# Performance work log

Measured on AMD Instinct MI355X. Metric: run time of the kernel, lower is better.

Reference implementation:

```python
import jax, jax.numpy as jnp
import numpy as np

B, C, H, W = 8, 64, 64, 64
CQK = C // 8

def setup_inputs() -> dict:
    key = jax.random.key(0)
    ks = jax.random.split(key, 8)
    s = 0.05
    return {
        "X": jax.random.normal(ks[0], (B, C, H, W), dtype=jnp.float32),
        "Wq": jax.random.normal(ks[1], (CQK, C), dtype=jnp.float32) * s,
        "bq": jax.random.normal(ks[2], (CQK,), dtype=jnp.float32) * s,
        "Wk": jax.random.normal(ks[3], (CQK, C), dtype=jnp.float32) * s,
        "bk": jax.random.normal(ks[4], (CQK,), dtype=jnp.float32) * s,
        "Wv": jax.random.normal(ks[5], (C, C), dtype=jnp.float32) * s,
        "bv": jax.random.normal(ks[6], (C,), dtype=jnp.float32) * s,
        "gamma": jax.random.normal(ks[7], (1,), dtype=jnp.float32) * 0.5,
    }

def reference(X, Wq, bq, Wk, bk, Wv, bv, gamma):
    b, c, h, w = X.shape
    n = h * w
    Xf = X.reshape(b, c, n)  # [B, C, N]
    # 1x1 convs == per-pixel linear over channels
    q = jnp.einsum('oc,bcn->bno', Wq, Xf) + bq            # [B, N, Cqk]
    k = jnp.einsum('oc,bcn->bon', Wk, Xf) + bk[:, None]    # [B, Cqk, N]
    v = jnp.einsum('oc,bcn->bon', Wv, Xf) + bv[:, None]    # [B, C, N]
    energy = jnp.einsum('bnd,bdm->bnm', q, k)              # [B, N, N] (no scale, as in source)
    attention = jax.nn.softmax(energy, axis=-1)
    out = jnp.einsum('bcn,bmn->bcm', v, attention)         # value @ attention^T
    out = out.reshape(b, c, h, w)
    return X + out * gamma[0]
```

## Files before the change

### kernel.cpp

```cpp
#include <hip/hip_runtime.h>
#include <hip/hip_bf16.h>

#define BB 8
#define CC 64
#define NN 4096
#define LOG2E 1.44269504088896340736f

typedef short bf16x8 __attribute__((ext_vector_type(8)));
typedef float f32x16 __attribute__((ext_vector_type(16)));
typedef unsigned int uint4v __attribute__((ext_vector_type(4)));

__device__ __forceinline__ unsigned cvt_pk_bf16(float lo, float hi) {
    unsigned r;
    asm("v_cvt_pk_bf16_f32 %0, %1, %2" : "=v"(r) : "v"(lo), "v"(hi));
    return r;
}

__device__ __forceinline__ float fast_exp2(float x) {
#if __has_builtin(__builtin_amdgcn_exp2f)
    return __builtin_amdgcn_exp2f(x);
#else
    return __builtin_exp2f(x);
#endif
}


__global__ __launch_bounds__(256) void qkv_kernel(
    const float* __restrict__ X,
    const float* __restrict__ Wq, const float* __restrict__ bq,
    const float* __restrict__ Wk, const float* __restrict__ bk,
    const float* __restrict__ Wv, const float* __restrict__ bv,
    unsigned short* __restrict__ qw, unsigned short* __restrict__ kfrag,
    unsigned short* __restrict__ vfrag)
{
    __shared__ float wbuf[64 * 16];
    __shared__ float bsh[16];
    __shared__ short vsh[16][264];

    const int t = threadIdx.x;
    const int grp = blockIdx.x % 5;
    const int tile = blockIdx.x / 5;
    const int b = tile >> 4;
    const int nb = (tile & 15) << 8;
    const int n = nb + t;

    if (grp == 0) {
        for (int i = t; i < 512; i += 256) {
            int o = i >> 6, c = i & 63;
            wbuf[c * 16 + o]     = Wq[i];
            wbuf[c * 16 + 8 + o] = Wk[i];
        }
        if (t < 8) { bsh[t] = bq[t]; bsh[8 + t] = bk[t]; }
    } else {
        const int cbase = (grp - 1) * 16;
        for (int i = t; i < 1024; i += 256) {
            int o = i >> 6, c = i & 63;
            wbuf[c * 16 + o] = Wv[(cbase + o) * 64 + c];
        }
        if (t < 16) bsh[t] = bv[cbase + t];
    }
    __syncthreads();

    float a[16];
    #pragma unroll
    for (int j = 0; j < 16; j++) a[j] = bsh[j];

    const float* xp = X + (size_t)b * CC * NN + n;
    for (int c = 0; c < 64; c++) {
        float xc = xp[(size_t)c * NN];
        const float4* w4 = (const float4*)&wbuf[c * 16];
        float4 w0 = w4[0], w1 = w4[1], w2 = w4[2], w3 = w4[3];
        a[0]  += w0.x * xc; a[1]  += w0.y * xc; a[2]  += w0.z * xc; a[3]  += w0.w * xc;
        a[4]  += w1.x * xc; a[5]  += w1.y * xc; a[6]  += w1.z * xc; a[7]  += w1.w * xc;
        a[8]  += w2.x * xc; a[9]  += w2.y * xc; a[10] += w2.z * xc; a[11] += w2.w * xc;
        a[12] += w3.x * xc; a[13] += w3.y * xc; a[14] += w3.z * xc; a[15] += w3.w * xc;
    }

    if (grp == 0) {
        alignas(16) __hip_bfloat16 qb8[8], kb8[8];
        #pragma unroll
        for (int d = 0; d < 8; d++) {
            qb8[d] = __float2bfloat16(a[d] * LOG2E);
            kb8[d] = __float2bfloat16(a[8 + d]);
        }
        const size_t g = (size_t)b * NN + n;
        *(int4*)(qw + g * 8) = *(const int4*)qb8;
        size_t kf = ((size_t)b * 128 + (n >> 5)) * 512;
        *(int4*)(kfrag + kf + (size_t)(n & 31) * 8) = *(const int4*)kb8;
        *(int4*)(kfrag + kf + (size_t)(32 + (n & 31)) * 8) = make_int4(0, 0, 0, 0);
    } else {
        const int cbase = (grp - 1) * 16;
        const int qb0 = cbase & 31, ct = cbase >> 5;
        #pragma unroll
        for (int j = 0; j < 16; j++)
            vsh[j][t] = __builtin_bit_cast(short, __float2bfloat16(a[j]));
        __syncthreads();
        #pragma unroll
        for (int rr = 0; rr < 2; ++rr) {
            int r = 2 * t + rr;
            int qq = r & 15, hh = (r >> 4) & 1, gg = (r >> 5) & 3, tau = r >> 7;
            int n0 = tau * 64 + gg * 16 + hh * 8;
            int4 val = *(const int4*)&vsh[qq][n0];
            int gtile = (nb >> 6) + tau;
            size_t dst = ((size_t)(b * 64 + gtile)) * 4096
                       + (size_t)(gg * 2 + ct) * 512
                       + (size_t)(32 * hh + qb0 + qq) * 8;
            *(int4*)(vfrag + dst) = val;
        }
    }
}

template<int KS, bool FUSE>
__global__ __launch_bounds__(256, 2) void attn_kernel(
    const unsigned short* __restrict__ qw,
    const unsigned short* __restrict__ kfrag,
    const unsigned short* __restrict__ vfrag,
    unsigned short* __restrict__ pout, float* __restrict__ pl,
    const float* __restrict__ X, const float* __restrict__ gamma,
    float* __restrict__ out)
{
    const int t = threadIdx.x;
    const int w = t >> 6, lane = t & 63;
    const int h = lane >> 5, q = lane & 31;

    const int nwg = gridDim.x;
    const int cpx = nwg >> 3;
    const int bid = (blockIdx.x & 7) * cpx + (blockIdx.x >> 3);

    const int qtile = bid & 15;
    const int b = (bid >> 4) & 7;
    const int ks = bid >> 7;

    const int qbase = qtile * 256 + w * 64;

    bf16x8 qfA = {}, qfB = {};
    if (h == 0) {
        qfA = *(const bf16x8*)(qw + ((size_t)b * NN + qbase + q) * 8);
        qfB = *(const bf16x8*)(qw + ((size_t)b * NN + qbase + 32 + q) * 8);
    }

    f32x16 accA0 = {}, accA1 = {}, accB0 = {}, accB1 = {};
    float lsumA = 0.f, lsumB = 0.f;

    const int NT = NN / KS / 64;
    const unsigned short* kb = kfrag + (size_t)b * 65536
                             + (size_t)ks * NT * 1024 + (size_t)lane * 8;
    const unsigned short* vbp = vfrag + (size_t)b * 262144
                              + (size_t)ks * NT * 4096 + (size_t)lane * 8;

    auto phase = [&](const f32x16& sA, const f32x16& sB,
                     bf16x8 va, bf16x8 vb2, bf16x8 vc, bf16x8 vd) {
        float pa[16], pb[16];
        #pragma unroll
        for (int r = 0; r < 16; ++r) { pa[r] = fast_exp2(sA[r]); pb[r] = fast_exp2(sB[r]); }
        {
            float a0 = 0.f, a1 = 0.f, b0 = 0.f, b1 = 0.f;
            #pragma unroll
            for (int r = 0; r < 8; ++r) {
                a0 += pa[r]; a1 += pa[8 + r];
                b0 += pb[r]; b1 += pb[8 + r];
            }
            lsumA += a0 + a1;
            lsumB += b0 + b1;
        }
        unsigned ka[8], kb2[8];
        #pragma unroll
        for (int j = 0; j < 8; ++j) {
            ka[j]  = cvt_pk_bf16(pa[2 * j], pa[2 * j + 1]);
            kb2[j] = cvt_pk_bf16(pb[2 * j], pb[2 * j + 1]);
        }
        __builtin_amdgcn_s_setprio(1);
        #pragma unroll
        for (int g2 = 0; g2 < 2; ++g2) {
            const unsigned* pga = &ka[4 * g2];
            auto ra = __builtin_amdgcn_permlane32_swap(pga[2], pga[0], false, false);
            auto rb = __builtin_amdgcn_permlane32_swap(pga[3], pga[1], false, false);
            uint4v bua = { ra[1], rb[1], ra[0], rb[0] };
            bf16x8 pfA = __builtin_bit_cast(bf16x8, bua);
            const unsigned* pgb = &kb2[4 * g2];
            auto rc = __builtin_amdgcn_permlane32_swap(pgb[2], pgb[0], false, false);
            auto rd = __builtin_amdgcn_permlane32_swap(pgb[3], pgb[1], false, false);
            uint4v bub = { rc[1], rd[1], rc[0], rd[0] };
            bf16x8 pfB = __builtin_bit_cast(bf16x8, bub);

            bf16x8 vx = g2 ? vc : va;
            bf16x8 vy = g2 ? vd : vb2;
            accA0 = __builtin_amdgcn_mfma_f32_32x32x16_bf16(vx, pfA, accA0, 0, 0, 0);
            accA1 = __builtin_amdgcn_mfma_f32_32x32x16_bf16(vy, pfA, accA1, 0, 0, 0);
            accB0 = __builtin_amdgcn_mfma_f32_32x32x16_bf16(vx, pfB, accB0, 0, 0, 0);
            accB1 = __builtin_amdgcn_mfma_f32_32x32x16_bf16(vy, pfB, accB1, 0, 0, 0);
        }
        __builtin_amdgcn_s_setprio(0);
    };

    bf16x8 kc0 = *(const bf16x8*)kb;
    bf16x8 kc1 = *(const bf16x8*)(kb + 512);

    for (int it = 0; it < NT; ++it) {
        const unsigned short* vp = vbp + (size_t)it * 4096;
        bf16x8 v0 = *(const bf16x8*)(vp);
        bf16x8 v1 = *(const bf16x8*)(vp + 512);
        bf16x8 v2 = *(const bf16x8*)(vp + 1024);
        bf16x8 v3 = *(const bf16x8*)(vp + 1536);
        bf16x8 v4 = *(const bf16x8*)(vp + 2048);
        bf16x8 v5 = *(const bf16x8*)(vp + 2560);
        bf16x8 v6 = *(const bf16x8*)(vp + 3072);
        bf16x8 v7 = *(const bf16x8*)(vp + 3584);

        const int nit = (it + 1 < NT) ? it + 1 : it;
        const unsigned short* knp = kb + (size_t)nit * 1024;
        bf16x8 kn0 = *(const bf16x8*)knp;
        bf16x8 kn1 = *(const bf16x8*)(knp + 512);

        {
            f32x16 sA = __builtin_amdgcn_mfma_f32_32x32x16_bf16(kc0, qfA, (f32x16){}, 0, 0, 0);
            f32x16 sB = __builtin_amdgcn_mfma_f32_32x32x16_bf16(kc0, qfB, (f32x16){}, 0, 0, 0);
            phase(sA, sB, v0, v1, v2, v3);
        }
        {
            f32x16 sA = __builtin_amdgcn_mfma_f32_32x32x16_bf16(kc1, qfA, (f32x16){}, 0, 0, 0);
            f32x16 sB = __builtin_amdgcn_mfma_f32_32x32x16_bf16(kc1, qfB, (f32x16){}, 0, 0, 0);
            phase(sA, sB, v4, v5, v6, v7);
        }
        kc0 = kn0;
        kc1 = kn1;
    }

    auto rsA = __builtin_amdgcn_permlane32_swap(__builtin_bit_cast(unsigned, lsumA),
                                                __builtin_bit_cast(unsigned, lsumA), false, false);
    float ltotA = __builtin_bit_cast(float, rsA[0]) + __builtin_bit_cast(float, rsA[1]);
    auto rsB = __builtin_amdgcn_permlane32_swap(__builtin_bit_cast(unsigned, lsumB),
                                                __builtin_bit_cast(unsigned, lsumB), false, false);
    float ltotB = __builtin_bit_cast(float, rsB[0]) + __builtin_bit_cast(float, rsB[1]);

    const float gm = FUSE ? gamma[0] : 0.f;

    #pragma unroll
    for (int sub = 0; sub < 2; ++sub) {
        const int n = qbase + sub * 32 + q;
        const float ltot = sub ? ltotB : ltotA;
        const f32x16& a0 = sub ? accB0 : accA0;
        const f32x16& a1 = sub ? accB1 : accA1;
        if (FUSE) {
            const float inv = 1.f / ltot;
            #pragma unroll
            for (int ct = 0; ct < 2; ++ct) {
                const f32x16& a = ct ? a1 : a0;
                #pragma unroll
                for (int r = 0; r < 16; ++r) {
                    int c = ct * 32 + (r & 3) + 8 * (r >> 2) + 4 * h;
                    size_t idx = ((size_t)(b * CC + c)) * NN + n;
                    out[idx] = X[idx] + gm * a[r] * inv;
                }
            }
        } else {
            unsigned short* po = pout + (size_t)ks * BB * CC * NN;
            #pragma unroll
            for (int ct = 0; ct < 2; ++ct) {
                const f32x16& a = ct ? a1 : a0;
                #pragma unroll
                for (int r = 0; r < 16; ++r) {
                    int c = ct * 32 + (r & 3) + 8 * (r >> 2) + 4 * h;
                    po[((size_t)(b * CC + c)) * NN + n] =
                        __builtin_bit_cast(unsigned short, __float2bfloat16(a[r]));
                }
            }
            if (h == 0) pl[((size_t)(ks * BB + b)) * NN + n] = ltot;
        }
    }
}

template<int KS>
__global__ __launch_bounds__(256) void combine_kernel(
    const unsigned short* __restrict__ pout, const float* __restrict__ pl,
    const float* __restrict__ X, const float* __restrict__ gamma,
    float* __restrict__ out)
{
    const int idx = blockIdx.x * 256 + threadIdx.x;
    const int n4 = idx & 1023;
    const int c  = (idx >> 10) & 63;
    const int b  = idx >> 16;
    const int n0 = n4 * 4;
    const float gm = gamma[0];
    const size_t base = ((size_t)(b * CC + c)) * NN + n0;

    float4 s = make_float4(0.f, 0.f, 0.f, 0.f);
    float4 L = make_float4(0.f, 0.f, 0.f, 0.f);
    #pragma unroll
    for (int ks = 0; ks < KS; ++ks) {
        ushort4 sv = *(const ushort4*)(pout + (size_t)ks * BB * CC * NN + base);
        float4 lv = *(const float4*)(pl + ((size_t)(ks * BB + b)) * NN + n0);
        s.x += __bfloat162float(__builtin_bit_cast(__hip_bfloat16, sv.x));
        s.y += __bfloat162float(__builtin_bit_cast(__hip_bfloat16, sv.y));
        s.z += __bfloat162float(__builtin_bit_cast(__hip_bfloat16, sv.z));
        s.w += __bfloat162float(__builtin_bit_cast(__hip_bfloat16, sv.w));
        L.x += lv.x; L.y += lv.y; L.z += lv.z; L.w += lv.w;
    }
    float4 x = *(const float4*)(X + base);
    float4 o;
    o.x = x.x + gm * s.x / L.x;
    o.y = x.y + gm * s.y / L.y;
    o.z = x.z + gm * s.z / L.z;
    o.w = x.w + gm * s.w / L.w;
    *(float4*)(out + base) = o;
}

extern "C" void kernel_launch(void* const* d_in, const int* in_sizes, int n_in,
                              void* d_out, int out_size, void* d_ws, size_t ws_size,
                              hipStream_t stream) {
    const float* X  = (const float*)d_in[0];
    const float* Wq = (const float*)d_in[1];
    const float* bq = (const float*)d_in[2];
    const float* Wk = (const float*)d_in[3];
    const float* bk = (const float*)d_in[4];
    const float* Wv = (const float*)d_in[5];
    const float* bv = (const float*)d_in[6];
    const float* gm = (const float*)d_in[7];
    float* out = (float*)d_out;

    unsigned short* qw    = (unsigned short*)d_ws;
    unsigned short* kfrag = qw + (size_t)BB * NN * 8;
    unsigned short* vfrag = kfrag + (size_t)BB * 128 * 512;
    unsigned short* pout  = vfrag + (size_t)BB * 64 * 4096;
    float* pl = (float*)(pout + (size_t)4 * BB * CC * NN);

    const size_t qkv_bytes = ((size_t)BB * NN * 8 + (size_t)BB * 128 * 512
                            + (size_t)BB * 64 * 4096) * 2;
    const size_t need4 = qkv_bytes + (size_t)4 * BB * CC * NN * 2 + (size_t)4 * BB * NN * 4;
    const size_t need2 = qkv_bytes + (size_t)2 * BB * CC * NN * 2 + (size_t)2 * BB * NN * 4;

    qkv_kernel<<<dim3(640), dim3(256), 0, stream>>>(X, Wq, bq, Wk, bk, Wv, bv, qw, kfrag, vfrag);

    if (ws_size >= need4) {
        attn_kernel<4, false><<<dim3(512), dim3(256), 0, stream>>>(
            qw, kfrag, vfrag, pout, pl, X, gm, out);
        combine_kernel<4><<<dim3((BB * CC * NN / 4) / 256), dim3(256), 0, stream>>>(
            pout, pl, X, gm, out);
    } else if (ws_size >= need2) {
        float* pl2 = (float*)(pout + (size_t)2 * BB * CC * NN);
        attn_kernel<2, false><<<dim3(256), dim3(256), 0, stream>>>(
            qw, kfrag, vfrag, pout, pl2, X, gm, out);
        combine_kernel<2><<<dim3((BB * CC * NN / 4) / 256), dim3(256), 0, stream>>>(
            pout, pl2, X, gm, out);
    } else {
        attn_kernel<1, true><<<dim3(128), dim3(256), 0, stream>>>(
            qw, kfrag, vfrag, nullptr, nullptr, X, gm, out);
    }
}
```

Baseline: 51.51 us.

## Split attention keys 8 ways, raise occupancy, and restructure the inner loop for fewer registers

Raises the key-split factor from 4 to 8, launching 1024 workgroups with a larger partial-output workspace, and drops the 2-way path in favour of an 8-way path. Launch bounds go from 2 to 3 waves per SIMD. The inner phase now loads its own K/V fragments and handles the A and B softmax halves one after another, with no K prefetch, to reduce live registers. The goal is more parallelism and better latency hiding across waves. The cost is a larger combine-kernel workload, more partial-output traffic, and no explicit K prefetch.

```diff
diff --git a/kernel.cpp b/kernel.cpp
--- a/kernel.cpp
+++ b/kernel.cpp
@@ -111,7 +111,7 @@
 }
 
 template<int KS, bool FUSE>
-__global__ __launch_bounds__(256, 2) void attn_kernel(
+__global__ __launch_bounds__(256, 3) void attn_kernel(
     const unsigned short* __restrict__ qw,
     const unsigned short* __restrict__ kfrag,
     const unsigned short* __restrict__ vfrag,
@@ -148,27 +148,39 @@
     const unsigned short* vbp = vfrag + (size_t)b * 262144
                               + (size_t)ks * NT * 4096 + (size_t)lane * 8;
 
-    auto phase = [&](const f32x16& sA, const f32x16& sB,
-                     bf16x8 va, bf16x8 vb2, bf16x8 vc, bf16x8 vd) {
-        float pa[16], pb[16];
-        #pragma unroll
-        for (int r = 0; r < 16; ++r) { pa[r] = fast_exp2(sA[r]); pb[r] = fast_exp2(sB[r]); }
+    auto phase = [&](const unsigned short* kp, const unsigned short* vp) {
+        bf16x8 kc = *(const bf16x8*)kp;
+        bf16x8 v0 = *(const bf16x8*)(vp);
+        bf16x8 v1 = *(const bf16x8*)(vp + 512);
+        bf16x8 v2 = *(const bf16x8*)(vp + 1024);
+        bf16x8 v3 = *(const bf16x8*)(vp + 1536);
+
+        unsigned ka[8], kb2[8];
         {
-            float a0 = 0.f, a1 = 0.f, b0 = 0.f, b1 = 0.f;
-            #pragma unroll
-            for (int r = 0; r < 8; ++r) {
-                a0 += pa[r]; a1 += pa[8 + r];
-                b0 += pb[r]; b1 += pb[8 + r];
-            }
+            f32x16 sA = __builtin_amdgcn_mfma_f32_32x32x16_bf16(kc, qfA, (f32x16){}, 0, 0, 0);
+            float pa[16];
+            #pragma unroll
+            for (int r = 0; r < 16; ++r) pa[r] = fast_exp2(sA[r]);
+            float a0 = 0.f, a1 = 0.f;
+            #pragma unroll
+            for (int r = 0; r < 8; ++r) { a0 += pa[r]; a1 += pa[8 + r]; }
             lsumA += a0 + a1;
+            #pragma unroll
+            for (int j = 0; j < 8; ++j) ka[j] = cvt_pk_bf16(pa[2 * j], pa[2 * j + 1]);
+        }
+        {
+            f32x16 sB = __builtin_amdgcn_mfma_f32_32x32x16_bf16(kc, qfB, (f32x16){}, 0, 0, 0);
+            float pb[16];
+            #pragma unroll
+            for (int r = 0; r < 16; ++r) pb[r] = fast_exp2(sB[r]);
+            float b0 = 0.f, b1 = 0.f;
+            #pragma unroll
+            for (int r = 0; r < 8; ++r) { b0 += pb[r]; b1 += pb[8 + r]; }
             lsumB += b0 + b1;
-        }
-        unsigned ka[8], kb2[8];
-        #pragma unroll
-        for (int j = 0; j < 8; ++j) {
-            ka[j]  = cvt_pk_bf16(pa[2 * j], pa[2 * j + 1]);
-            kb2[j] = cvt_pk_bf16(pb[2 * j], pb[2 * j + 1]);
-        }
+            #pragma unroll
+            for (int j = 0; j < 8; ++j) kb2[j] = cvt_pk_bf16(pb[2 * j], pb[2 * j + 1]);
+        }
+
         __builtin_amdgcn_s_setprio(1);
         #pragma unroll
         for (int g2 = 0; g2 < 2; ++g2) {
@@ -183,8 +195,8 @@
             uint4v bub = { rc[1], rd[1], rc[0], rd[0] };
             bf16x8 pfB = __builtin_bit_cast(bf16x8, bub);
 
-            bf16x8 vx = g2 ? vc : va;
-            bf16x8 vy = g2 ? vd : vb2;
+            bf16x8 vx = g2 ? v2 : v0;
+            bf16x8 vy = g2 ? v3 : v1;
             accA0 = __builtin_amdgcn_mfma_f32_32x32x16_bf16(vx, pfA, accA0, 0, 0, 0);
             accA1 = __builtin_amdgcn_mfma_f32_32x32x16_bf16(vy, pfA, accA1, 0, 0, 0);
             accB0 = __builtin_amdgcn_mfma_f32_32x32x16_bf16(vx, pfB, accB0, 0, 0, 0);
@@ -193,37 +205,11 @@
         __builtin_amdgcn_s_setprio(0);
     };
 
-    bf16x8 kc0 = *(const bf16x8*)kb;
-    bf16x8 kc1 = *(const bf16x8*)(kb + 512);
-
     for (int it = 0; it < NT; ++it) {
+        const unsigned short* kp = kb + (size_t)it * 1024;
         const unsigned short* vp = vbp + (size_t)it * 4096;
-        bf16x8 v0 = *(const bf16x8*)(vp);
-        bf16x8 v1 = *(const bf16x8*)(vp + 512);
-        bf16x8 v2 = *(const bf16x8*)(vp + 1024);
-        bf16x8 v3 = *(const bf16x8*)(vp + 1536);
-        bf16x8 v4 = *(const bf16x8*)(vp + 2048);
-        bf16x8 v5 = *(const bf16x8*)(vp + 2560);
-        bf16x8 v6 = *(const bf16x8*)(vp + 3072);
-        bf16x8 v7 = *(const bf16x8*)(vp + 3584);
-
-        const int nit = (it + 1 < NT) ? it + 1 : it;
-        const unsigned short* knp = kb + (size_t)nit * 1024;
-        bf16x8 kn0 = *(const bf16x8*)knp;
-        bf16x8 kn1 = *(const bf16x8*)(knp + 512);
-
-        {
-            f32x16 sA = __builtin_amdgcn_mfma_f32_32x32x16_bf16(kc0, qfA, (f32x16){}, 0, 0, 0);
-            f32x16 sB = __builtin_amdgcn_mfma_f32_32x32x16_bf16(kc0, qfB, (f32x16){}, 0, 0, 0);
-            phase(sA, sB, v0, v1, v2, v3);
-        }
-        {
-            f32x16 sA = __builtin_amdgcn_mfma_f32_32x32x16_bf16(kc1, qfA, (f32x16){}, 0, 0, 0);
-            f32x16 sB = __builtin_amdgcn_mfma_f32_32x32x16_bf16(kc1, qfB, (f32x16){}, 0, 0, 0);
-            phase(sA, sB, v4, v5, v6, v7);
-        }
-        kc0 = kn0;
-        kc1 = kn1;
+        phase(kp, vp);
+        phase(kp + 512, vp + 2048);
     }
 
     auto rsA = __builtin_amdgcn_permlane32_swap(__builtin_bit_cast(unsigned, lsumA),
@@ -322,26 +308,26 @@
     unsigned short* kfrag = qw + (size_t)BB * NN * 8;
     unsigned short* vfrag = kfrag + (size_t)BB * 128 * 512;
     unsigned short* pout  = vfrag + (size_t)BB * 64 * 4096;
-    float* pl = (float*)(pout + (size_t)4 * BB * CC * NN);
+    float* pl = (float*)(pout + (size_t)8 * BB * CC * NN);
 
     const size_t qkv_bytes = ((size_t)BB * NN * 8 + (size_t)BB * 128 * 512
                             + (size_t)BB * 64 * 4096) * 2;
+    const size_t need8 = qkv_bytes + (size_t)8 * BB * CC * NN * 2 + (size_t)8 * BB * NN * 4;
     const size_t need4 = qkv_bytes + (size_t)4 * BB * CC * NN * 2 + (size_t)4 * BB * NN * 4;
-    const size_t need2 = qkv_bytes + (size_t)2 * BB * CC * NN * 2 + (size_t)2 * BB * NN * 4;
 
     qkv_kernel<<<dim3(640), dim3(256), 0, stream>>>(X, Wq, bq, Wk, bk, Wv, bv, qw, kfrag, vfrag);
 
-    if (ws_size >= need4) {
+    if (ws_size >= need8) {
+        attn_kernel<8, false><<<dim3(1024), dim3(256), 0, stream>>>(
+            qw, kfrag, vfrag, pout, pl, X, gm, out);
+        combine_kernel<8><<<dim3((BB * CC * NN / 4) / 256), dim3(256), 0, stream>>>(
+            pout, pl, X, gm, out);
+    } else if (ws_size >= need4) {
+        float* pl4 = (float*)(pout + (size_t)4 * BB * CC * NN);
         attn_kernel<4, false><<<dim3(512), dim3(256), 0, stream>>>(
-            qw, kfrag, vfrag, pout, pl, X, gm, out);
+            qw, kfrag, vfrag, pout, pl4, X, gm, out);
         combine_kernel<4><<<dim3((BB * CC * NN / 4) / 256), dim3(256), 0, stream>>>(
-            pout, pl, X, gm, out);
-    } else if (ws_size >= need2) {
-        float* pl2 = (float*)(pout + (size_t)2 * BB * CC * NN);
-        attn_kernel<2, false><<<dim3(256), dim3(256), 0, stream>>>(
-            qw, kfrag, vfrag, pout, pl2, X, gm, out);
-        combine_kernel<2><<<dim3((BB * CC * NN / 4) / 256), dim3(256), 0, stream>>>(
-            pout, pl2, X, gm, out);
+            pout, pl4, X, gm, out);
     } else {
         attn_kernel<1, true><<<dim3(128), dim3(256), 0, stream>>>(
             qw, kfrag, vfrag, nullptr, nullptr, X, gm, out);
```

Result: slower. 56.20 us (+9.1%).
